# Optimization experiments

Measured on AMD Instinct MI355X. Metric: run time of the kernel, lower is better.

The kernel has to match this reference:

```python
import jax, jax.numpy as jnp
import numpy as np

B, S, D, H, FF = 16, 384, 768, 12, 3072
DH = D // H


def layer_norm(x, g, b, eps=1e-5):
    m = jnp.mean(x, axis=-1, keepdims=True)
    v = jnp.mean((x - m) ** 2, axis=-1, keepdims=True)
    return (x - m) * jax.lax.rsqrt(v + eps) * g + b


def setup_inputs() -> dict:
    key = jax.random.key(0)
    ks = jax.random.split(key, 12)
    s = 0.02
    return {
        "x": jax.random.normal(ks[0], (B, S, D), dtype=jnp.float32),
        "pe": jax.random.normal(ks[1], (2 * S - 1, D), dtype=jnp.float32) * s,  # relative-position table for offsets -(S-1)..(S-1)
        "Wq": jax.random.normal(ks[2], (D, D), dtype=jnp.float32) * s,
        "Wk": jax.random.normal(ks[3], (D, D), dtype=jnp.float32) * s,
        "Wv": jax.random.normal(ks[4], (D, D), dtype=jnp.float32) * s,
        "Wr": jax.random.normal(ks[5], (D, D), dtype=jnp.float32) * s,
        "u": jax.random.normal(ks[6], (H, DH), dtype=jnp.float32) * s,  # content bias (Transformer-XL)
        "v": jax.random.normal(ks[7], (H, DH), dtype=jnp.float32) * s,  # position bias
        "Wo": jax.random.normal(ks[8], (D, D), dtype=jnp.float32) * s,  # attn_ff output projection
        "ln1_g": jnp.ones((D,), dtype=jnp.float32),
        "ln1_b": jnp.zeros((D,), dtype=jnp.float32),
        "ln2_g": jnp.ones((D,), dtype=jnp.float32),
        "ln2_b": jnp.zeros((D,), dtype=jnp.float32),
        "W1": jax.random.normal(ks[9], (D, FF), dtype=jnp.float32) * s,
        "b1": jnp.zeros((FF,), dtype=jnp.float32),
        "W2": jax.random.normal(ks[10], (FF, D), dtype=jnp.float32) * s,
        "b2": jnp.zeros((D,), dtype=jnp.float32),
    }


def reference(x, pe, Wq, Wk, Wv, Wr, u, v, Wo, ln1_g, ln1_b, ln2_g, ln2_b, W1, b1, W2, b2):
    # --- relative-position multi-head self-attention (FLAT / Transformer-XL style) ---
    q = (x @ Wq).reshape(B, S, H, DH)
    k = (x @ Wk).reshape(B, S, H, DH)
    val = (x @ Wv).reshape(B, S, H, DH)
    # project relative table once, then gather per (i, j) offset
    r = (pe @ Wr).reshape(2 * S - 1, H, DH)
    idx = jnp.arange(S)[:, None] - jnp.arange(S)[None, :] + (S - 1)  # [S,S], offset i-j shifted
    rel = r[idx]  # [S,S,H,DH]
    A_C = jnp.einsum("bqhd,bkhd->bhqk", q + u, k)
    B_D = jnp.einsum("bqhd,qkhd->bhqk", q + v, rel)
    scores = (A_C + B_D) * (1.0 / np.sqrt(DH))  # scaled=True
    p = jax.nn.softmax(scores, axis=-1)
    attn = jnp.einsum("bhqk,bkhd->bqhd", p, val).reshape(B, S, D) @ Wo
    # layer_postprocess_sequence = 'an': add residual, then layernorm
    x1 = layer_norm(x + attn, ln1_g, ln1_b)
    # --- FFN (relu) with 'an' postprocess ---
    ff = jax.nn.relu(x1 @ W1 + b1) @ W2 + b2
    return layer_norm(x1 + ff, ln2_g, ln2_b)
```

## Files before the change

### kernel.cpp

```cpp
#include <hip/hip_runtime.h>

typedef unsigned short u16;
typedef __attribute__((ext_vector_type(8))) short short8;
typedef __attribute__((ext_vector_type(4))) float floatx4;

#define B_  16
#define S_  384
#define D_  768
#define H_  12
#define DH_ 64
#define FF_ 3072

__device__ __forceinline__ float b2f(u16 h) { return __uint_as_float(((unsigned)h) << 16); }
__device__ __forceinline__ u16 f2b(float f) {
  unsigned u = __float_as_uint(f);
  u += 0x7fffu + ((u >> 16) & 1u);
  return (u16)(u >> 16);
}

__device__ __forceinline__ void gload16(const u16* g, u16* l) {
  __builtin_amdgcn_global_load_lds(
      (const __attribute__((address_space(1))) unsigned int*)g,
      (__attribute__((address_space(3))) unsigned int*)l, 16, 0, 0);
}

__global__ __launch_bounds__(256) void fill_sentinel(u16* out, int n) {
  int i = blockIdx.x * 256 + threadIdx.x;
  if (i < n) out[i] = 0x42DE;
}

__device__ __forceinline__ int detect_flag(const u16* x, int tid, int* sh) {
  const unsigned e = (x[tid] >> 7) & 0xFFu;
  const unsigned long long m = __ballot(e >= 0xC0u);
  if ((tid & 63) == 0) sh[tid >> 6] = (m != 0ull) ? 1 : 0;
  __syncthreads();
  return sh[0] | sh[1] | sh[2] | sh[3];
}

struct TP { const void* src[7]; u16* dst[7]; };
__global__ __launch_bounds__(256) void preamble_all(
    TP tp, const void* x, const void* pe,
    const void* b1, const void* ub, const void* vb, const void* b2,
    const void* g1, const void* be1, const void* g2, const void* be2,
    u16* xb, u16* peb,
    u16* b1c, u16* ubc, u16* vbc, u16* b2c,
    u16* g1c, u16* be1c, u16* g2c, u16* be2c, int* flag_ws) {
  __shared__ u16 t[32][33];
  __shared__ int fl[4];
  const int tid = threadIdx.x;
  const int f32 = detect_flag((const u16*)x, tid, fl);
  const int id = blockIdx.x;
  if (id == 0 && tid == 0) *flag_ws = f32;

  if (id < 7488) {
    int w, tt, R, C, bc, br;
    if (id < 2880)      { w = id / 576; tt = id % 576;  R = 768;  C = 768;  bc = (tt % 24) * 32; br = (tt / 24) * 32; }
    else if (id < 5184) { w = 5;        tt = id - 2880; R = 768;  C = 3072; bc = (tt % 96) * 32; br = (tt / 96) * 32; }
    else                { w = 6;        tt = id - 5184; R = 3072; C = 768;  bc = (tt % 24) * 32; br = (tt / 24) * 32; }
    const void* in = tp.src[w];
    u16* out = tp.dst[w];
    const int tx = tid & 31, ty = tid >> 5;
    for (int i = ty; i < 32; i += 8) {
      const size_t idx = (size_t)(br + i) * C + bc + tx;
      t[i][tx] = f32 ? f2b(((const float*)in)[idx]) : ((const u16*)in)[idx];
    }
    __syncthreads();
    for (int i = ty; i < 32; i += 8) out[(size_t)(bc + i) * R + br + tx] = t[tx][i];
  } else if (id < 12096) {
    const int i = (id - 7488) * 256 + tid;
    if (i < B_ * S_ * D_ / 4) {
      if (f32) {
        const float4 f = ((const float4*)x)[i];
        ushort4 o;
        o.x = f2b(f.x); o.y = f2b(f.y); o.z = f2b(f.z); o.w = f2b(f.w);
        ((ushort4*)xb)[i] = o;
      } else {
        ((ushort4*)xb)[i] = ((const ushort4*)x)[i];
      }
    }
  } else if (id < 12672) {
    const int i = (id - 12096) * 256 + tid;
    if (i < (2 * S_ - 1) * D_ / 4) {
      if (f32) {
        const float4 f = ((const float4*)pe)[i];
        ushort4 o;
        o.x = f2b(f.x); o.y = f2b(f.y); o.z = f2b(f.z); o.w = f2b(f.w);
        ((ushort4*)peb)[i] = o;
      } else {
        ((ushort4*)peb)[i] = ((const ushort4*)pe)[i];
      }
    }
  } else {
    const int i = (id - 12672) * 256 + tid;
    if (i < 8448) {
      const void* s; u16* d; int off;
      if (i < 3072) { s = b1; d = b1c; off = i; }
      else {
        const int r = i - 3072, sg = r / 768; off = r - sg * 768;
        switch (sg) {
          case 0: s = ub;  d = ubc;  break;
          case 1: s = vb;  d = vbc;  break;
          case 2: s = b2;  d = b2c;  break;
          case 3: s = g1;  d = g1c;  break;
          case 4: s = be1; d = be1c; break;
          case 5: s = g2;  d = g2c;  break;
          default: s = be2; d = be2c; break;
        }
      }
      d[off] = f32 ? f2b(((const float*)s)[off]) : ((const u16*)s)[off];
    }
  }
}

enum { F_BIAS = 1, F_RELU = 2, F_RES = 4 };

template <int TM, int TN, int WM, int WN, int FLAGS>
__global__ __launch_bounds__(256) void gemm3(
    const u16* __restrict__ A, const u16* __restrict__ Bt,
    u16* __restrict__ out0, const u16* __restrict__ bias0,
    const u16* __restrict__ res, int M, int N, int K) {
  constexpr int WAVES_M = TM / WM;
  constexpr int MT = WM / 16, NT = WN / 16;
  constexpr int NI = (TM + TN) / 64;
  static_assert((TM / WM) * (TN / WN) == 4, "4 waves");
  __shared__ u16 SM[2][(TM + TN) * 32];

  const int m0 = blockIdx.y * TM;
  const int n0 = blockIdx.x * TN;
  const int tid = threadIdx.x;
  const int wid = tid >> 6, lane = tid & 63;
  const int wm = (wid % WAVES_M) * WM, wn = (wid / WAVES_M) * WN;
  const int lm = lane & 15, quad = lane >> 4;

  floatx4 acc[MT][NT];
#pragma unroll
  for (int i = 0; i < MT; ++i)
#pragma unroll
    for (int j = 0; j < NT; ++j) acc[i][j] = (floatx4){0.f, 0.f, 0.f, 0.f};

  const u16* srcs[NI];
  int ldso[NI];
#pragma unroll
  for (int i = 0; i < NI; ++i) {
    const int j = wid + 4 * i;
    const int r = j * 16 + (lane >> 2);
    const int q = (lane & 3) ^ ((r >> 1) & 3);
    const u16* p;
    if (r < TM) {
      int ga = m0 + r;
      if (ga > M - 1) ga = M - 1;
      p = A + (size_t)ga * K + q * 8;
    } else {
      p = Bt + (size_t)(n0 + r - TM) * K + q * 8;
    }
    srcs[i] = p;
    ldso[i] = j * 512;
  }
  const int slot = (quad ^ ((lm >> 1) & 3)) * 8;
  int aoff[MT], boff[NT];
#pragma unroll
  for (int t = 0; t < MT; ++t) aoff[t] = (wm + t * 16 + lm) * 32 + slot;
#pragma unroll
  for (int t = 0; t < NT; ++t) boff[t] = (TM + wn + t * 16 + lm) * 32 + slot;

#pragma unroll
  for (int i = 0; i < NI; ++i) gload16(srcs[i], &SM[0][ldso[i]]);
  __syncthreads();

  int buf = 0;
  for (int k0 = 0; k0 < K; k0 += 32, buf ^= 1) {
    if (k0 + 32 < K) {
      const int koff = (k0 + 32);
#pragma unroll
      for (int i = 0; i < NI; ++i) gload16(srcs[i] + koff, &SM[buf ^ 1][ldso[i]]);
    }
    short8 af[MT], bf[NT];
#pragma unroll
    for (int t = 0; t < MT; ++t) af[t] = *(const short8*)(&SM[buf][aoff[t]]);
#pragma unroll
    for (int t = 0; t < NT; ++t) bf[t] = *(const short8*)(&SM[buf][boff[t]]);
#pragma unroll
    for (int tm = 0; tm < MT; ++tm)
#pragma unroll
      for (int tn = 0; tn < NT; ++tn)
        acc[tm][tn] = __builtin_amdgcn_mfma_f32_16x16x32_bf16(af[tm], bf[tn], acc[tm][tn], 0, 0, 0);
    __syncthreads();
  }

#pragma unroll
  for (int tm = 0; tm < MT; ++tm) {
#pragma unroll
    for (int tn = 0; tn < NT; ++tn) {
      const int gcol = n0 + wn + tn * 16 + lm;
#pragma unroll
      for (int r = 0; r < 4; ++r) {
        const int grow = m0 + wm + tm * 16 + quad * 4 + r;
        if (grow >= M) continue;
        float val = acc[tm][tn][r];
        if (FLAGS & F_BIAS) val += b2f(bias0[gcol]);
        if (FLAGS & F_RES) val += b2f(res[(size_t)grow * N + gcol]);
        if (FLAGS & F_RELU) val = fmaxf(val, 0.f);
        out0[(size_t)grow * N + gcol] = f2b(val);
      }
    }
  }
}

__global__ __launch_bounds__(256) void gemm_qkv_rp(
    const u16* __restrict__ xb, const u16* __restrict__ wqkv,
    const u16* __restrict__ peb, const u16* __restrict__ wtr,
    u16* __restrict__ qu, u16* __restrict__ qv,
    u16* __restrict__ kbo, u16* __restrict__ vto, u16* __restrict__ rbo,
    const u16* __restrict__ ubias, const u16* __restrict__ vbias) {
  constexpr int TM = 128, TN = 128, WM = 64, WN = 64;
  constexpr int MT = 4, NT = 4, NI = 4;
  __shared__ u16 SM[2][(TM + TN) * 32];

  const int id = blockIdx.x;
  const int qkv = (id < 864) ? 1 : 0;
  int bx, by, M, N;
  const u16 *A, *Bt;
  if (qkv) { bx = id % 18; by = id / 18; M = B_ * S_; N = 2304; A = xb; Bt = wqkv; }
  else     { const int t2 = id - 864; bx = t2 % 6; by = t2 / 6; M = 767; N = 768; A = peb; Bt = wtr; }
  const int K = 768;
  const int m0 = by * TM, n0 = bx * TN;
  const int tid = threadIdx.x;
  const int wid = tid >> 6, lane = tid & 63;
  const int wm = (wid & 1) * WM, wn = (wid >> 1) * WN;
  const int lm = lane & 15, quad = lane >> 4;

  floatx4 acc[MT][NT];
#pragma unroll
  for (int i = 0; i < MT; ++i)
#pragma unroll
    for (int j = 0; j < NT; ++j) acc[i][j] = (floatx4){0.f, 0.f, 0.f, 0.f};

  const u16* srcs[NI];
  int ldso[NI];
#pragma unroll
  for (int i = 0; i < NI; ++i) {
    const int j = wid + 4 * i;
    const int r = j * 16 + (lane >> 2);
    const int q = (lane & 3) ^ ((r >> 1) & 3);
    const u16* p;
    if (r < TM) {
      int ga = m0 + r;
      if (ga > M - 1) ga = M - 1;
      p = A + (size_t)ga * K + q * 8;
    } else {
      p = Bt + (size_t)(n0 + r - TM) * K + q * 8;
    }
    srcs[i] = p;
    ldso[i] = j * 512;
  }
  const int slot = (quad ^ ((lm >> 1) & 3)) * 8;
  int aoff[MT], boff[NT];
#pragma unroll
  for (int t = 0; t < MT; ++t) aoff[t] = (wm + t * 16 + lm) * 32 + slot;
#pragma unroll
  for (int t = 0; t < NT; ++t) boff[t] = (TM + wn + t * 16 + lm) * 32 + slot;

#pragma unroll
  for (int i = 0; i < NI; ++i) gload16(srcs[i], &SM[0][ldso[i]]);
  __syncthreads();

  int buf = 0;
  for (int k0 = 0; k0 < K; k0 += 32, buf ^= 1) {
    if (k0 + 32 < K) {
      const int koff = (k0 + 32);
#pragma unroll
      for (int i = 0; i < NI; ++i) gload16(srcs[i] + koff, &SM[buf ^ 1][ldso[i]]);
    }
    short8 af[MT], bf[NT];
#pragma unroll
    for (int t = 0; t < MT; ++t) af[t] = *(const short8*)(&SM[buf][aoff[t]]);
#pragma unroll
    for (int t = 0; t < NT; ++t) bf[t] = *(const short8*)(&SM[buf][boff[t]]);
#pragma unroll
    for (int tm = 0; tm < MT; ++tm)
#pragma unroll
      for (int tn = 0; tn < NT; ++tn)
        acc[tm][tn] = __builtin_amdgcn_mfma_f32_16x16x32_bf16(af[tm], bf[tn], acc[tm][tn], 0, 0, 0);
    __syncthreads();
  }

  if (!qkv) {
#pragma unroll
    for (int tm = 0; tm < MT; ++tm)
#pragma unroll
      for (int tn = 0; tn < NT; ++tn) {
        const int gcol = n0 + wn + tn * 16 + lm;
#pragma unroll
        for (int r = 0; r < 4; ++r) {
          const int grow = m0 + wm + tm * 16 + quad * 4 + r;
          if (grow < M) rbo[(size_t)grow * 768 + gcol] = f2b(acc[tm][tn][r]);
        }
      }
    return;
  }
  const int region = n0 / 768;
  if (region == 2) {
    u16* wbuf = &SM[0][0] + wid * 1088;
    const int bb = (m0 + wm) / S_;
    const int sbase = (m0 + wm) % S_;
    const int cl = lane >> 2, sc = (lane & 3) * 16;
#pragma unroll
    for (int tn = 0; tn < NT; ++tn) {
#pragma unroll
      for (int tm = 0; tm < MT; ++tm)
#pragma unroll
        for (int r = 0; r < 4; ++r)
          wbuf[(tm * 16 + quad * 4 + r) * 17 + lm] = f2b(acc[tm][tn][r]);
      short8 s0, s1;
#pragma unroll
      for (int j = 0; j < 8; ++j) s0[j] = (short)wbuf[(sc + j) * 17 + cl];
#pragma unroll
      for (int j = 0; j < 8; ++j) s1[j] = (short)wbuf[(sc + 8 + j) * 17 + cl];
      const int cglob = n0 - 1536 + wn + tn * 16 + cl;
      u16* dst = vto + ((size_t)(bb * D_ + cglob)) * S_ + sbase + sc;
      *(short8*)dst = s0;
      *(short8*)(dst + 8) = s1;
    }
    return;
  }
#pragma unroll
  for (int tm = 0; tm < MT; ++tm) {
#pragma unroll
    for (int tn = 0; tn < NT; ++tn) {
      const int gcol = n0 + wn + tn * 16 + lm;
      const int c = gcol - region * 768;
#pragma unroll
      for (int r = 0; r < 4; ++r) {
        const int grow = m0 + wm + tm * 16 + quad * 4 + r;
        const float val = acc[tm][tn][r];
        if (region == 0) {
          qu[(size_t)grow * 768 + c] = f2b(val + b2f(ubias[c]));
          qv[(size_t)grow * 768 + c] = f2b(val + b2f(vbias[c]));
        } else {
          kbo[(size_t)grow * 768 + c] = f2b(val);
        }
      }
    }
  }
}

__global__ __launch_bounds__(512, 4) void attn_kernel(
    const u16* __restrict__ qu, const u16* __restrict__ qv,
    const u16* __restrict__ kb, const u16* __restrict__ vt,
    const u16* __restrict__ rb, u16* __restrict__ attn) {
  __shared__ float scA[32 * 396];
  __shared__ u16 Eb[32 * 424];
  __shared__ float rsum[32];

  const int id = blockIdx.x;
  const int g = id >> 3;
  const int qt = g % 12;
  const int bh = (id & 7) + 8 * (g / 12);
  const int b = bh / H_, h = bh % H_;
  const int i0 = qt * 32;
  const int tid = threadIdx.x, wid = tid >> 6, lane = tid & 63;
  const int lm = lane & 15, quad = lane >> 4;

  const size_t qr0 = ((size_t)(b * S_ + i0 + lm)) * D_ + h * DH_;
  const size_t qr1 = qr0 + (size_t)16 * D_;
  const short8 qv0a = *(const short8*)(qv + qr0 + quad * 8);
  const short8 qv0b = *(const short8*)(qv + qr0 + 32 + quad * 8);
  const short8 qv1a = *(const short8*)(qv + qr1 + quad * 8);
  const short8 qv1b = *(const short8*)(qv + qr1 + 32 + quad * 8);
  const short8 qu0a = *(const short8*)(qu + qr0 + quad * 8);
  const short8 qu0b = *(const short8*)(qu + qr0 + 32 + quad * 8);
  const short8 qu1a = *(const short8*)(qu + qr1 + quad * 8);
  const short8 qu1b = *(const short8*)(qu + qr1 + 32 + quad * 8);

  for (int u = wid; u < 50; u += 8) {
    if (u < 26) {
      const int m = u;
      int t = i0 + 16 * m + lm;
      if (t > 766) t = 766;
      const u16* p = rb + (size_t)t * D_ + h * DH_;
      const short8 b0 = *(const short8*)(p + quad * 8);
      const short8 b1 = *(const short8*)(p + 32 + quad * 8);
      if (m <= 24) {
        floatx4 e = (floatx4){0.f, 0.f, 0.f, 0.f};
        e = __builtin_amdgcn_mfma_f32_16x16x32_bf16(qv0a, b0, e, 0, 0, 0);
        e = __builtin_amdgcn_mfma_f32_16x16x32_bf16(qv0b, b1, e, 0, 0, 0);
#pragma unroll
        for (int r = 0; r < 4; ++r) Eb[(quad * 4 + r) * 424 + 16 * m + lm] = f2b(e[r]);
      }
      if (m >= 1) {
        floatx4 e = (floatx4){0.f, 0.f, 0.f, 0.f};
        e = __builtin_amdgcn_mfma_f32_16x16x32_bf16(qv1a, b0, e, 0, 0, 0);
        e = __builtin_amdgcn_mfma_f32_16x16x32_bf16(qv1b, b1, e, 0, 0, 0);
#pragma unroll
        for (int r = 0; r < 4; ++r) Eb[(16 + quad * 4 + r) * 424 + 16 * (m - 1) + lm] = f2b(e[r]);
      }
    } else {
      const int j = u - 26;
      const u16* p = kb + ((size_t)(b * S_ + j * 16 + lm)) * D_ + h * DH_;
      const short8 b0 = *(const short8*)(p + quad * 8);
      const short8 b1 = *(const short8*)(p + 32 + quad * 8);
      floatx4 e0 = (floatx4){0.f, 0.f, 0.f, 0.f};
      e0 = __builtin_amdgcn_mfma_f32_16x16x32_bf16(qu0a, b0, e0, 0, 0, 0);
      e0 = __builtin_amdgcn_mfma_f32_16x16x32_bf16(qu0b, b1, e0, 0, 0, 0);
      floatx4 e1 = (floatx4){0.f, 0.f, 0.f, 0.f};
      e1 = __builtin_amdgcn_mfma_f32_16x16x32_bf16(qu1a, b0, e1, 0, 0, 0);
      e1 = __builtin_amdgcn_mfma_f32_16x16x32_bf16(qu1b, b1, e1, 0, 0, 0);
#pragma unroll
      for (int r = 0; r < 4; ++r) {
        scA[(quad * 4 + r) * 396 + j * 16 + lm] = e0[r];
        scA[(16 + quad * 4 + r) * 396 + j * 16 + lm] = e1[r];
      }
    }
  }
  __syncthreads();

  u16* p16 = (u16*)scA;
  {
    const int row = wid * 4 + quad;
    const int rbase = row * 424 + (row & 15) + 383;
    float v[24];
    float lmax = -1e30f;
#pragma unroll
    for (int cc = 0; cc < 24; ++cc) {
      const int c = lm + cc * 16;
      const float s = (scA[row * 396 + c] + b2f(Eb[rbase - c])) * 0.125f;
      v[cc] = s;
      lmax = fmaxf(lmax, s);
    }
#pragma unroll
    for (int m = 1; m < 16; m <<= 1) lmax = fmaxf(lmax, __shfl_xor(lmax, m));
    float lsum = 0.f;
#pragma unroll
    for (int cc = 0; cc < 24; ++cc) {
      const float e = __expf(v[cc] - lmax);
      p16[row * 792 + lm + cc * 16] = f2b(e);
      lsum += e;
    }
#pragma unroll
    for (int m = 1; m < 16; m <<= 1) lsum += __shfl_xor(lsum, m);
    if (lm == 0) rsum[row] = lsum;
  }
  __syncthreads();

  {
    const int rg = wid & 1, nt = wid >> 1;
    floatx4 o = (floatx4){0.f, 0.f, 0.f, 0.f};
    const size_t vbase = ((size_t)(b * D_ + h * DH_ + nt * 16 + lm)) * S_;
    const int pbase = (rg * 16 + lm) * 792;
#pragma unroll
    for (int kk = 0; kk < 12; ++kk) {
      const short8 af = *(const short8*)(&p16[pbase + kk * 32 + quad * 8]);
      const short8 bv = *(const short8*)(vt + vbase + kk * 32 + quad * 8);
      o = __builtin_amdgcn_mfma_f32_16x16x32_bf16(af, bv, o, 0, 0, 0);
    }
#pragma unroll
    for (int r = 0; r < 4; ++r) {
      const int row = rg * 16 + quad * 4 + r;
      attn[((size_t)(b * S_ + i0 + row)) * D_ + h * DH_ + nt * 16 + lm] =
          f2b(o[r] / rsum[row]);
    }
  }
}

__global__ __launch_bounds__(256) void ln_kernel(const u16* __restrict__ y,
                                                 const u16* __restrict__ g,
                                                 const u16* __restrict__ bb,
                                                 void* __restrict__ outv,
                                                 const int* __restrict__ flag, int dual) {
  const int row = blockIdx.x * 4 + (threadIdx.x >> 6);
  const int lane = threadIdx.x & 63;
  const u16* yr = y + (size_t)row * D_;
  float vbuf[12], s = 0.f, s2 = 0.f;
#pragma unroll
  for (int i = 0; i < 12; ++i) {
    const float x = b2f(yr[lane + i * 64]);
    vbuf[i] = x;
    s += x;
    s2 += x * x;
  }
#pragma unroll
  for (int off = 32; off; off >>= 1) {
    s += __shfl_down(s, off);
    s2 += __shfl_down(s2, off);
  }
  s = __shfl(s, 0);
  s2 = __shfl(s2, 0);
  const float mean = s * (1.f / 768.f);
  const float var = s2 * (1.f / 768.f) - mean * mean;
  const float inv = rsqrtf(var + 1e-5f);
  const int f32out = dual && *flag;
#pragma unroll
  for (int i = 0; i < 12; ++i) {
    const int c = lane + i * 64;
    const float val = (vbuf[i] - mean) * inv * b2f(g[c]) + b2f(bb[c]);
    if (f32out) ((float*)outv)[(size_t)row * D_ + c] = val;
    else ((u16*)outv)[(size_t)row * D_ + c] = f2b(val);
  }
}

extern "C" void kernel_launch(void* const* d_in, const int* in_sizes, int n_in,
                              void* d_out, int out_size, void* d_ws, size_t ws_size,
                              hipStream_t stream) {
  const void* x    = d_in[0];
  const void* pe   = d_in[1];
  const void* Wq   = d_in[2];
  const void* Wk   = d_in[3];
  const void* Wv   = d_in[4];
  const void* Wr   = d_in[5];
  const void* ub   = d_in[6];
  const void* vb   = d_in[7];
  const void* Wo   = d_in[8];
  const void* ln1g = d_in[9];
  const void* ln1b = d_in[10];
  const void* ln2g = d_in[11];
  const void* ln2b = d_in[12];
  const void* W1   = d_in[13];
  const void* b1   = d_in[14];
  const void* W2   = d_in[15];
  const void* b2   = d_in[16];
  char* ws = (char*)d_ws;

  constexpr size_t O_W   = 0;
  constexpr size_t O_SM  = 15335424;
  constexpr size_t O_XB  = 15368192;
  constexpr size_t O_QU  = 24805376;
  constexpr size_t O_QV  = 34242560;
  constexpr size_t O_KB  = 43679744;
  constexpr size_t O_VT  = 53116928;
  constexpr size_t O_RB  = 62554112;
  constexpr size_t NEEDED = 63733760;

  if (ws_size < NEEDED) {
    fill_sentinel<<<(out_size + 255) / 256, 256, 0, stream>>>((u16*)d_out, out_size);
    return;
  }

  int* flag = (int*)(ws + O_SM);
  u16* ubc  = (u16*)(ws + O_SM + 128);
  u16* vbc  = (u16*)(ws + O_SM + 1664);
  u16* b1c  = (u16*)(ws + O_SM + 3200);
  u16* b2c  = (u16*)(ws + O_SM + 9344);
  u16* g1c  = (u16*)(ws + O_SM + 10880);
  u16* be1c = (u16*)(ws + O_SM + 12416);
  u16* g2c  = (u16*)(ws + O_SM + 13952);
  u16* be2c = (u16*)(ws + O_SM + 15488);

  u16* wtq = (u16*)(ws + O_W);
  u16* wtk = wtq + (size_t)D_ * D_;
  u16* wtv = wtk + (size_t)D_ * D_;
  u16* wtr = wtv + (size_t)D_ * D_;
  u16* wto = wtr + (size_t)D_ * D_;
  u16* wt1 = wto + (size_t)D_ * D_;
  u16* wt2 = wt1 + (size_t)D_ * FF_;

  u16* xb  = (u16*)(ws + O_XB);
  u16* quB = (u16*)(ws + O_QU);
  u16* qvB = (u16*)(ws + O_QV);
  u16* kbB = (u16*)(ws + O_KB);
  u16* vtB = (u16*)(ws + O_VT);
  u16* rbB = (u16*)(ws + O_RB);
  u16* peb = (u16*)d_out;
  u16* atB = (u16*)d_out;
  u16* y1B = xb;
  u16* x1B = (u16*)(ws + O_VT);
  u16* ffB = xb;
  u16* y2B = x1B;

  TP tp;
  tp.src[0] = Wq; tp.src[1] = Wk; tp.src[2] = Wv; tp.src[3] = Wr; tp.src[4] = Wo;
  tp.src[5] = W1; tp.src[6] = W2;
  tp.dst[0] = wtq; tp.dst[1] = wtk; tp.dst[2] = wtv; tp.dst[3] = wtr; tp.dst[4] = wto;
  tp.dst[5] = wt1; tp.dst[6] = wt2;

  preamble_all<<<12705, 256, 0, stream>>>(tp, x, pe, b1, ub, vb, b2, ln1g, ln1b,
                                          ln2g, ln2b, xb, peb, b1c, ubc, vbc, b2c,
                                          g1c, be1c, g2c, be2c, flag);
  gemm_qkv_rp<<<900, 256, 0, stream>>>(xb, wtq, peb, wtr, quB, qvB, kbB, vtB, rbB,
                                       ubc, vbc);
  attn_kernel<<<2304, 512, 0, stream>>>(quB, qvB, kbB, vtB, rbB, atB);
  gemm3<64, 128, 32, 64, F_RES><<<dim3(6, 96), 256, 0, stream>>>(
      atB, wto, y1B, nullptr, xb, B_ * S_, D_, D_);
  ln_kernel<<<B_ * S_ / 4, 256, 0, stream>>>(y1B, g1c, be1c, x1B, flag, 0);
  gemm3<128, 128, 64, 64, F_BIAS | F_RELU><<<dim3(24, 48), 256, 0, stream>>>(
      x1B, wt1, ffB, b1c, nullptr, B_ * S_, FF_, D_);
  gemm3<64, 128, 32, 64, F_BIAS | F_RES><<<dim3(6, 96), 256, 0, stream>>>(
      ffB, wt2, y2B, b2c, x1B, B_ * S_, D_, FF_);
  ln_kernel<<<B_ * S_ / 4, 256, 0, stream>>>(y2B, g2c, be2c, d_out, flag, 1);
}
```

Baseline: 428.1 us.

## Store content scores as bf16 in LDS, raise attention occupancy, prefetch next tile

The attention kernel now keeps the q·k content scores as bf16 in a smaller shared buffer instead of fp32. This roughly halves that buffer's LDS footprint, and the launch bound is raised from 4 to 6 blocks per CU to match. The score loop also software-prefetches the next iteration's rel/key operand rows into registers, so global load latency overlaps the current MFMAs. In exchange, the content scores lose precision before softmax, and the extra registers could pressure the higher occupancy target.

New measurement: 419.0 us. 1.02x faster.

```diff
diff --git a/kernel.cpp b/kernel.cpp
--- a/kernel.cpp
+++ b/kernel.cpp
@@ -344,11 +344,11 @@
   }
 }
 
-__global__ __launch_bounds__(512, 4) void attn_kernel(
+__global__ __launch_bounds__(512, 6) void attn_kernel(
     const u16* __restrict__ qu, const u16* __restrict__ qv,
     const u16* __restrict__ kb, const u16* __restrict__ vt,
     const u16* __restrict__ rb, u16* __restrict__ attn) {
-  __shared__ float scA[32 * 396];
+  __shared__ u16 scB[32 * 408];
   __shared__ u16 Eb[32 * 424];
   __shared__ float rsum[32];
 
@@ -372,14 +372,30 @@
   const short8 qu1a = *(const short8*)(qu + qr1 + quad * 8);
   const short8 qu1b = *(const short8*)(qu + qr1 + 32 + quad * 8);
 
+  short8 b0, b1;
+  {
+    const int t = i0 + 16 * wid + lm;
+    const u16* p = rb + (size_t)t * D_ + h * DH_ + quad * 8;
+    b0 = *(const short8*)p;
+    b1 = *(const short8*)(p + 32);
+  }
   for (int u = wid; u < 50; u += 8) {
+    short8 n0 = b0, n1 = b1;
+    const int un = u + 8;
+    if (un < 50) {
+      const u16* pn;
+      if (un < 26) {
+        int t = i0 + 16 * un + lm;
+        if (t > 766) t = 766;
+        pn = rb + (size_t)t * D_ + h * DH_ + quad * 8;
+      } else {
+        pn = kb + ((size_t)(b * S_ + (un - 26) * 16 + lm)) * D_ + h * DH_ + quad * 8;
+      }
+      n0 = *(const short8*)pn;
+      n1 = *(const short8*)(pn + 32);
+    }
     if (u < 26) {
       const int m = u;
-      int t = i0 + 16 * m + lm;
-      if (t > 766) t = 766;
-      const u16* p = rb + (size_t)t * D_ + h * DH_;
-      const short8 b0 = *(const short8*)(p + quad * 8);
-      const short8 b1 = *(const short8*)(p + 32 + quad * 8);
       if (m <= 24) {
         floatx4 e = (floatx4){0.f, 0.f, 0.f, 0.f};
         e = __builtin_amdgcn_mfma_f32_16x16x32_bf16(qv0a, b0, e, 0, 0, 0);
@@ -396,9 +412,6 @@
       }
     } else {
       const int j = u - 26;
-      const u16* p = kb + ((size_t)(b * S_ + j * 16 + lm)) * D_ + h * DH_;
-      const short8 b0 = *(const short8*)(p + quad * 8);
-      const short8 b1 = *(const short8*)(p + 32 + quad * 8);
       floatx4 e0 = (floatx4){0.f, 0.f, 0.f, 0.f};
       e0 = __builtin_amdgcn_mfma_f32_16x16x32_bf16(qu0a, b0, e0, 0, 0, 0);
       e0 = __builtin_amdgcn_mfma_f32_16x16x32_bf16(qu0b, b1, e0, 0, 0, 0);
@@ -407,14 +420,15 @@
       e1 = __builtin_amdgcn_mfma_f32_16x16x32_bf16(qu1b, b1, e1, 0, 0, 0);
 #pragma unroll
       for (int r = 0; r < 4; ++r) {
-        scA[(quad * 4 + r) * 396 + j * 16 + lm] = e0[r];
-        scA[(16 + quad * 4 + r) * 396 + j * 16 + lm] = e1[r];
-      }
-    }
+        scB[(quad * 4 + r) * 408 + j * 16 + lm] = f2b(e0[r]);
+        scB[(16 + quad * 4 + r) * 408 + j * 16 + lm] = f2b(e1[r]);
+      }
+    }
+    b0 = n0;
+    b1 = n1;
   }
   __syncthreads();
 
-  u16* p16 = (u16*)scA;
   {
     const int row = wid * 4 + quad;
     const int rbase = row * 424 + (row & 15) + 383;
@@ -423,7 +437,7 @@
 #pragma unroll
     for (int cc = 0; cc < 24; ++cc) {
       const int c = lm + cc * 16;
-      const float s = (scA[row * 396 + c] + b2f(Eb[rbase - c])) * 0.125f;
+      const float s = (b2f(scB[row * 408 + c]) + b2f(Eb[rbase - c])) * 0.125f;
       v[cc] = s;
       lmax = fmaxf(lmax, s);
     }
@@ -433,7 +447,7 @@
 #pragma unroll
     for (int cc = 0; cc < 24; ++cc) {
       const float e = __expf(v[cc] - lmax);
-      p16[row * 792 + lm + cc * 16] = f2b(e);
+      scB[row * 408 + lm + cc * 16] = f2b(e);
       lsum += e;
     }
 #pragma unroll
@@ -446,10 +460,10 @@
     const int rg = wid & 1, nt = wid >> 1;
     floatx4 o = (floatx4){0.f, 0.f, 0.f, 0.f};
     const size_t vbase = ((size_t)(b * D_ + h * DH_ + nt * 16 + lm)) * S_;
-    const int pbase = (rg * 16 + lm) * 792;
+    const int pbase = (rg * 16 + lm) * 408;
 #pragma unroll
     for (int kk = 0; kk < 12; ++kk) {
-      const short8 af = *(const short8*)(&p16[pbase + kk * 32 + quad * 8]);
+      const short8 af = *(const short8*)(&scB[pbase + kk * 32 + quad * 8]);
       const short8 bv = *(const short8*)(vt + vbase + kk * 32 + quad * 8);
       o = __builtin_amdgcn_mfma_f32_16x16x32_bf16(af, bv, o, 0, 0, 0);
     }
```
